# Optimization experiments

Measured on AMD Instinct MI355X. Metric: run time of the kernel, lower is better.

## Reference

```python
import jax, jax.numpy as jnp
import numpy as np
import math

HIDDEN = 1024
NUM_HEADS = 16
HEAD_DIM = HIDDEN // NUM_HEADS
B, S = 4, 1024


def setup_inputs() -> dict:
    key = jax.random.key(0)
    ks = jax.random.split(key, 16)
    sd = 1.0 / math.sqrt(HIDDEN)
    inp = {
        "x": jax.random.normal(ks[0], (B, S, HIDDEN), jnp.float32),
        "spikes": jax.random.uniform(ks[1], (B, S, HIDDEN), jnp.float32),
        "membrane_potential": jax.random.normal(ks[2], (B, S, HIDDEN), jnp.float32),
        "Wq": jax.random.normal(ks[3], (HIDDEN, HIDDEN), jnp.float32) * sd,
        "bq": jnp.zeros((HIDDEN,), jnp.float32),
        "Wk": jax.random.normal(ks[4], (HIDDEN, HIDDEN), jnp.float32) * sd,
        "bk": jnp.zeros((HIDDEN,), jnp.float32),
        "Wv": jax.random.normal(ks[5], (HIDDEN, HIDDEN), jnp.float32) * sd,
        "bv": jnp.zeros((HIDDEN,), jnp.float32),
        "Wo": jax.random.normal(ks[6], (HIDDEN, HIDDEN), jnp.float32) * sd,
        "bo": jnp.zeros((HIDDEN,), jnp.float32),
        "tau_decay": jnp.ones((NUM_HEADS,), jnp.float32) * 10.0,
        "Wg": jax.random.normal(ks[7], (HIDDEN, 2 * HIDDEN), jnp.float32) * sd,
        "bg": jnp.zeros((HIDDEN,), jnp.float32),
    }
    return inp


def _heads(t):  # [B,S,H] -> [B,nH,S,hd]
    Bv, Sv, _ = t.shape
    return t.reshape(Bv, Sv, NUM_HEADS, HEAD_DIM).transpose(0, 2, 1, 3)


def reference(x, spikes, membrane_potential, Wq, bq, Wk, bk, Wv, bv, Wo, bo, tau_decay, Wg, bg):
    scale = 1.0 / math.sqrt(HEAD_DIM)
    q = _heads(x @ Wq.T + bq)
    k = _heads(x @ Wk.T + bk)
    v = _heads(x @ Wv.T + bv)

    # raw scores [B,nH,S,S]
    scores = jnp.einsum('bhqd,bhkd->bhqk', q, k) * scale

    # per-head exponential temporal decay mask [nH,S,S]
    times = jnp.arange(S, dtype=jnp.float32)
    tdiff = jnp.abs(times[:, None] - times[None, :])  # [S,S]
    tmask = jnp.exp(-tdiff[None] / tau_decay[:, None, None])
    scores = scores * tmask[None]

    # spike correlation term
    sm = _heads(spikes)
    spike_attn = jnp.einsum('bhqd,bhkd->bhqk', sm, sm) * scale
    scores = scores * (1.0 + spike_attn)

    # membrane gating of V
    v = v * jax.nn.sigmoid(_heads(membrane_potential))

    probs = jax.nn.softmax(scores, axis=-1)
    context = jnp.einsum('bhqk,bhkd->bhqd', probs, v)
    context = context.transpose(0, 2, 1, 3).reshape(B, S, HIDDEN)

    # dendritic gate
    gate_in = jnp.concatenate([context, membrane_potential], axis=-1)
    gate = jax.nn.sigmoid(gate_in @ Wg.T + bg)
    context = context * gate

    return context @ Wo.T + bo
```

## Files before the change

kernel.cpp:

```cpp
#include <hip/hip_runtime.h>
#include <math.h>
#include <stdint.h>

namespace {

typedef __attribute__((ext_vector_type(8))) short s8v;
typedef __attribute__((ext_vector_type(4))) float f4v;
typedef unsigned short u16;

__device__ __forceinline__ float fexp2(float x) {
  return __builtin_amdgcn_exp2f(x);
}

__device__ __forceinline__ u16 f2bf(float f) {
  union { float f; uint32_t u; } v; v.f = f;
  uint32_t r = v.u + 0x7fffu + ((v.u >> 16) & 1u);
  return (u16)(r >> 16);
}
__device__ __forceinline__ float bf2f(u16 h) {
  union { uint32_t u; float f; } v; v.u = ((uint32_t)h) << 16;
  return v.f;
}
__device__ __forceinline__ uint32_t pk2r(float a, float b) {
  return (uint32_t)f2bf(a) | ((uint32_t)f2bf(b) << 16);
}
__device__ __forceinline__ uint32_t pk2p(float a, float b) {
  union { float f; uint32_t u; } x, y; x.f = a; y.f = b;
  return __builtin_amdgcn_perm(y.u + 0x8000u, x.u + 0x8000u, 0x07060302u);
}
__device__ __forceinline__ float sigmoidf_(float x) { return 1.0f / (1.0f + __expf(-x)); }

__device__ __forceinline__ void gload16(const u16* g, u16* l) {
  __builtin_amdgcn_global_load_lds(
      (const __attribute__((address_space(1))) void*)g,
      (__attribute__((address_space(3))) void*)l, 16, 0, 0);
}

struct CvtJob { const float* src; u16* dst; };
struct CvtArgs { CvtJob j[18]; };

__global__ __launch_bounds__(256) void cvt_kernel(CvtArgs a) {
  const CvtJob jb = a.j[blockIdx.y];
  const int i = blockIdx.x * 256 + threadIdx.x;
  const float4 v = ((const float4*)jb.src)[i];
  uint2 pk;
  pk.x = pk2r(v.x, v.y);
  pk.y = pk2r(v.z, v.w);
  ((uint2*)jb.dst)[i] = pk;
}

__global__ __launch_bounds__(256) void qkv_gemm(
    const u16* __restrict__ xb,
    const u16* __restrict__ Wqb, const u16* __restrict__ Wkb, const u16* __restrict__ Wvb,
    const float* __restrict__ bq, const float* __restrict__ bk, const float* __restrict__ bv,
    const float* __restrict__ mem,
    u16* __restrict__ Qb, u16* __restrict__ Kb, u16* __restrict__ Vt) {
  __shared__ u16 as_[8192], bs_[8192];
  const int t = threadIdx.x;
  const int nb = blockIdx.x, mb = blockIdx.y;
  const int sel = nb >> 3;
  const u16* W = sel == 0 ? Wqb : (sel == 1 ? Wkb : Wvb);
  const float* bias = sel == 0 ? bq : (sel == 1 ? bk : bv);
  const int m0 = mb * 128, n0 = (nb & 7) * 128;
  const f4v fz = {0.f, 0.f, 0.f, 0.f};
  f4v acc[4][4];
#pragma unroll
  for (int i = 0; i < 4; ++i)
#pragma unroll
    for (int j = 0; j < 4; ++j) acc[i][j] = fz;

  const int l = t & 63, w = t >> 6, wm = w >> 1, wn = w & 1;
  const int lr = l & 15, lq = l >> 4;
  const int rx = lr & 7;
  const int srow = t >> 3;
  const int scol = ((t & 7) ^ (srow & 7)) * 8;

#define QKV_STAGE(k0)                                                          \
  {                                                                            \
    const int kk_ = (k0);                                                      \
    _Pragma("unroll") for (int u = 0; u < 4; ++u) {                            \
      gload16(xb + (size_t)(m0 + u * 32 + srow) * 1024 + kk_ + scol,           \
              as_ + u * 2048 + t * 8);                                         \
      gload16(W + (size_t)(n0 + u * 32 + srow) * 1024 + kk_ + scol,            \
              bs_ + u * 2048 + t * 8);                                         \
    }                                                                          \
  }

  QKV_STAGE(0);

  if (sel < 2) {
    for (int c = 0; c < 16; ++c) {
      __syncthreads();
      s8v af[2][4], bf[2][4];
#pragma unroll
      for (int ks = 0; ks < 2; ++ks) {
        const int co = ((ks * 4 + lq) ^ rx) * 8;
#pragma unroll
        for (int mi = 0; mi < 4; ++mi)
          af[ks][mi] = *(const s8v*)(as_ + (wm * 64 + mi * 16 + lr) * 64 + co);
#pragma unroll
        for (int ni = 0; ni < 4; ++ni)
          bf[ks][ni] = *(const s8v*)(bs_ + (wn * 64 + ni * 16 + lr) * 64 + co);
      }
      __syncthreads();
      if (c < 15) QKV_STAGE((c + 1) << 6);
#pragma unroll
      for (int ks = 0; ks < 2; ++ks)
#pragma unroll
        for (int mi = 0; mi < 4; ++mi)
#pragma unroll
          for (int ni = 0; ni < 4; ++ni)
            acc[mi][ni] = __builtin_amdgcn_mfma_f32_16x16x32_bf16(
                bf[ks][ni], af[ks][mi], acc[mi][ni], 0, 0, 0);
    }
    u16* dst = (sel == 0) ? Qb : Kb;
#pragma unroll
    for (int mi = 0; mi < 4; ++mi)
#pragma unroll
      for (int ni = 0; ni < 4; ++ni) {
        const int m = m0 + wm * 64 + mi * 16 + lr;
        const int nb4 = n0 + wn * 64 + ni * 16 + lq * 4;
        const float4 b4 = *(const float4*)&bias[nb4];
        uint2 pk;
        pk.x = pk2r(acc[mi][ni][0] + b4.x, acc[mi][ni][1] + b4.y);
        pk.y = pk2r(acc[mi][ni][2] + b4.z, acc[mi][ni][3] + b4.w);
        *(uint2*)(dst + (size_t)m * 1024 + nb4) = pk;
      }
  } else {
    for (int c = 0; c < 16; ++c) {
      __syncthreads();
      s8v af[2][4], bf[2][4];
#pragma unroll
      for (int ks = 0; ks < 2; ++ks) {
        const int co = ((ks * 4 + lq) ^ rx) * 8;
#pragma unroll
        for (int mi = 0; mi < 4; ++mi)
          af[ks][mi] = *(const s8v*)(as_ + (wm * 64 + mi * 16 + lr) * 64 + co);
#pragma unroll
        for (int ni = 0; ni < 4; ++ni)
          bf[ks][ni] = *(const s8v*)(bs_ + (wn * 64 + ni * 16 + lr) * 64 + co);
      }
      __syncthreads();
      if (c < 15) QKV_STAGE((c + 1) << 6);
#pragma unroll
      for (int ks = 0; ks < 2; ++ks)
#pragma unroll
        for (int mi = 0; mi < 4; ++mi)
#pragma unroll
          for (int ni = 0; ni < 4; ++ni)
            acc[mi][ni] = __builtin_amdgcn_mfma_f32_16x16x32_bf16(
                af[ks][mi], bf[ks][ni], acc[mi][ni], 0, 0, 0);
    }
    const int b = m0 >> 10;
#pragma unroll
    for (int mi = 0; mi < 4; ++mi)
#pragma unroll
      for (int ni = 0; ni < 4; ++ni) {
        const int mrow = m0 + wm * 64 + mi * 16 + lq * 4;
        const int ncol = n0 + wn * 64 + ni * 16 + lr;
        const int h = ncol >> 6, d = ncol & 63;
        const float bi = bias[ncol];
        float tv[4];
#pragma unroll
        for (int r = 0; r < 4; ++r)
          tv[r] = (acc[mi][ni][r] + bi) * sigmoidf_(mem[(size_t)(mrow + r) * 1024 + ncol]);
        const int s = mrow & 1023;
        uint2 pk;
        pk.x = pk2r(tv[0], tv[1]);
        pk.y = pk2r(tv[2], tv[3]);
        *(uint2*)(Vt + ((size_t)((b * 16 + h) * 64 + d)) * 1024 + s) = pk;
      }
  }
#undef QKV_STAGE
}

template <int MODE>
__global__ __launch_bounds__(256) void gemm64(
    const u16* __restrict__ Ab, const u16* __restrict__ A2b,
    const u16* __restrict__ W, const float* __restrict__ bias,
    u16* __restrict__ outb, float* __restrict__ outf, int K) {
  __shared__ u16 as_[4096], bs_[8192];
  const int t = threadIdx.x, l = t & 63, w = t >> 6;
  const int wm = w >> 1, wn = w & 1, lr = l & 15, lq = l >> 4;
  const int m0 = blockIdx.y * 64, n0 = blockIdx.x * 128;
  const f4v fz = {0.f, 0.f, 0.f, 0.f};
  f4v acc[2][4];
#pragma unroll
  for (int i = 0; i < 2; ++i)
#pragma unroll
    for (int j = 0; j < 4; ++j) acc[i][j] = fz;
  const int rx = lr & 7;
  const int srow = t >> 3;
  const int scol = ((t & 7) ^ (srow & 7)) * 8;
  const int nc = K >> 6;

#define G64_STAGE(k0)                                                          \
  {                                                                            \
    const int kk_ = (k0);                                                      \
    const u16* Ae_ = Ab;                                                       \
    int ka_ = kk_;                                                             \
    if (MODE == 1 && kk_ >= 1024) { Ae_ = A2b; ka_ = kk_ - 1024; }             \
    _Pragma("unroll") for (int u = 0; u < 2; ++u)                              \
        gload16(Ae_ + (size_t)(m0 + u * 32 + srow) * 1024 + ka_ + scol,        \
                as_ + u * 2048 + t * 8);                                       \
    _Pragma("unroll") for (int u = 0; u < 4; ++u)                              \
        gload16(W + (size_t)(n0 + u * 32 + srow) * K + kk_ + scol,             \
                bs_ + u * 2048 + t * 8);                                       \
  }

  G64_STAGE(0);
  for (int c = 0; c < nc; ++c) {
    __syncthreads();
    s8v af[2][2], bf[2][4];
#pragma unroll
    for (int ks = 0; ks < 2; ++ks) {
      const int co = ((ks * 4 + lq) ^ rx) * 8;
#pragma unroll
      for (int mi = 0; mi < 2; ++mi)
        af[ks][mi] = *(const s8v*)(as_ + (wm * 32 + mi * 16 + lr) * 64 + co);
#pragma unroll
      for (int ni = 0; ni < 4; ++ni)
        bf[ks][ni] = *(const s8v*)(bs_ + (wn * 64 + ni * 16 + lr) * 64 + co);
    }
    __syncthreads();
    if (c + 1 < nc) G64_STAGE((c + 1) << 6);
#pragma unroll
    for (int ks = 0; ks < 2; ++ks)
#pragma unroll
      for (int mi = 0; mi < 2; ++mi)
#pragma unroll
        for (int ni = 0; ni < 4; ++ni)
          acc[mi][ni] = __builtin_amdgcn_mfma_f32_16x16x32_bf16(
              bf[ks][ni], af[ks][mi], acc[mi][ni], 0, 0, 0);
  }
#undef G64_STAGE

#pragma unroll
  for (int mi = 0; mi < 2; ++mi)
#pragma unroll
    for (int ni = 0; ni < 4; ++ni) {
      const int m = m0 + wm * 32 + mi * 16 + lr;
      const int nb4 = n0 + wn * 64 + ni * 16 + lq * 4;
      const float4 b4 = *(const float4*)&bias[nb4];
      if (MODE == 0) {
        float4 o;
        o.x = acc[mi][ni][0] + b4.x; o.y = acc[mi][ni][1] + b4.y;
        o.z = acc[mi][ni][2] + b4.z; o.w = acc[mi][ni][3] + b4.w;
        *(float4*)(outf + (size_t)m * 1024 + nb4) = o;
      } else {
        const uint2 a2 = *(const uint2*)(Ab + (size_t)m * 1024 + nb4);
        float cx[4] = {bf2f((u16)(a2.x & 0xffff)), bf2f((u16)(a2.x >> 16)),
                       bf2f((u16)(a2.y & 0xffff)), bf2f((u16)(a2.y >> 16))};
        float g[4];
        g[0] = cx[0] * sigmoidf_(acc[mi][ni][0] + b4.x);
        g[1] = cx[1] * sigmoidf_(acc[mi][ni][1] + b4.y);
        g[2] = cx[2] * sigmoidf_(acc[mi][ni][2] + b4.z);
        g[3] = cx[3] * sigmoidf_(acc[mi][ni][3] + b4.w);
        uint2 pk;
        pk.x = pk2r(g[0], g[1]);
        pk.y = pk2r(g[2], g[3]);
        *(uint2*)(outb + (size_t)m * 1024 + nb4) = pk;
      }
    }
}

__global__ __launch_bounds__(256) void attn_mfma(
    const u16* __restrict__ Qb, const u16* __restrict__ Kb,
    const u16* __restrict__ SPb, const u16* __restrict__ Vt,
    const float* __restrict__ tau, u16* __restrict__ CTXb) {
  __shared__ u16 kbuf[8192], skbuf[8192], vbuf[8192];
  __shared__ u16 pbuf[4][1024];
  const int t = threadIdx.x, l = t & 63, w = t >> 6;
  const int lr = l & 15, lq = l >> 4;
  const int pid = blockIdx.x;
  const int g = (pid & 7) + 8 * (pid >> 7);
  const int qt = (pid >> 3) & 15;
  const int h = g & 15, b = g >> 4;

  const float c2 = 1.44269504088896f / tau[h];
  const float K0 = 0.125f * 1.44269504088896f;
  float cNR[4][4], cNRi[4][4];
#pragma unroll
  for (int ni = 0; ni < 4; ++ni)
#pragma unroll
    for (int r = 0; r < 4; ++r) {
      const float d = c2 * (float)(ni * 16 + lq * 4 + r);
      cNR[ni][r]  = fexp2(d);
      cNRi[ni][r] = fexp2(-d);
    }

  s8v qf[2], sf[2];
  {
    const size_t base = ((size_t)(b * 1024 + qt * 64 + w * 16 + lr)) * 1024 + h * 64 + lq * 8;
    qf[0] = *(const s8v*)(Qb + base);
    qf[1] = *(const s8v*)(Qb + base + 32);
    sf[0] = *(const s8v*)(SPb + base);
    sf[1] = *(const s8v*)(SPb + base + 32);
  }
  const s8v ones = {0x3F80, 0x3F80, 0x3F80, 0x3F80, 0x3F80, 0x3F80, 0x3F80, 0x3F80};

  const f4v fz = {0.f, 0.f, 0.f, 0.f};
  f4v oacc[4], osum = fz;
#pragma unroll
  for (int i = 0; i < 4; ++i) oacc[i] = fz;

  const int iqw = qt * 64 + w * 16;
  const int srow = t >> 3;
  const int csw = ((t & 7) ^ (srow & 7)) * 8;
  const int rx = lr & 7;
  u16* pw = pbuf[w];

  auto stage = [&](int jc2, int pp) {
    const int j0s = jc2 * 64;
    const int lo = pp * 4096;
    const size_t kg = ((size_t)(b * 1024 + j0s + srow)) * 1024 + h * 64 + csw;
    gload16(Kb + kg, kbuf + lo + t * 8);
    gload16(Kb + kg + 32 * 1024, kbuf + lo + 2048 + t * 8);
    gload16(SPb + kg, skbuf + lo + t * 8);
    gload16(SPb + kg + 32 * 1024, skbuf + lo + 2048 + t * 8);
    const size_t vg = ((size_t)((b * 16 + h) * 64 + srow)) * 1024 + j0s + csw;
    gload16(Vt + vg, vbuf + lo + t * 8);
    gload16(Vt + vg + 32 * 1024, vbuf + lo + 2048 + t * 8);
  };

  stage(0, 0);
  int pp = 0;
  for (int jc = 0; jc < 16; ++jc) {
    const int j0 = jc * 64;
    __syncthreads();
    if (jc < 15) stage(jc + 1, pp ^ 1);
    const int lo = pp * 4096;

    f4v sa[4], ssa[4];
#pragma unroll
    for (int ni = 0; ni < 4; ++ni) { sa[ni] = fz; ssa[ni] = fz; }
#pragma unroll
    for (int ks = 0; ks < 2; ++ks) {
#pragma unroll
      for (int ni = 0; ni < 4; ++ni) {
        const int off = lo + (ni * 16 + lr) * 64 + (((ks * 4 + lq) ^ rx) * 8);
        const s8v kf = *(const s8v*)(kbuf + off);
        sa[ni] = __builtin_amdgcn_mfma_f32_16x16x32_bf16(kf, qf[ks], sa[ni], 0, 0, 0);
        const s8v skf = *(const s8v*)(skbuf + off);
        ssa[ni] = __builtin_amdgcn_mfma_f32_16x16x32_bf16(skf, sf[ks], ssa[ni], 0, 0, 0);
      }
    }

    const int D0 = iqw - j0;
    float pv[4][4];
    if (jc < qt) {
      const float EA = K0 * fexp2(-c2 * (float)(D0 + lr));
#pragma unroll
      for (int ni = 0; ni < 4; ++ni)
#pragma unroll
        for (int r = 0; r < 4; ++r) {
          const float t1 = fmaf(ssa[ni][r], 0.125f, 1.0f);
          pv[ni][r] = fexp2(sa[ni][r] * (cNR[ni][r] * EA) * t1);
        }
    } else if (jc > qt) {
      const float EAi = K0 * fexp2(c2 * (float)(D0 + lr));
#pragma unroll
      for (int ni = 0; ni < 4; ++ni)
#pragma unroll
        for (int r = 0; r < 4; ++r) {
          const float t1 = fmaf(ssa[ni][r], 0.125f, 1.0f);
          pv[ni][r] = fexp2(sa[ni][r] * (cNRi[ni][r] * EAi) * t1);
        }
    } else {
      const float EA  = K0 * fexp2(-c2 * (float)(D0 + lr));
      const float EAi = K0 * fexp2(c2 * (float)(D0 + lr));
#pragma unroll
      for (int ni = 0; ni < 4; ++ni)
#pragma unroll
        for (int r = 0; r < 4; ++r) {
          const int jloc = ni * 16 + lq * 4 + r;
          const float f = (D0 + lr >= jloc) ? cNR[ni][r] * EA : cNRi[ni][r] * EAi;
          const float t1 = fmaf(ssa[ni][r], 0.125f, 1.0f);
          pv[ni][r] = fexp2(sa[ni][r] * f * t1);
        }
    }

#pragma unroll
    for (int ni = 0; ni < 4; ++ni) {
      const int phys = (ni * 2 + (lq >> 1)) ^ rx;
      uint2 p2;
      p2.x = pk2p(pv[ni][0], pv[ni][1]);
      p2.y = pk2p(pv[ni][2], pv[ni][3]);
      *(uint2*)(pw + lr * 64 + phys * 8 + (lq & 1) * 4) = p2;
    }

#pragma unroll
    for (int ks = 0; ks < 2; ++ks) {
      const s8v pf = *(const s8v*)(pw + lr * 64 + (((ks * 4 + lq) ^ rx) * 8));
      osum = __builtin_amdgcn_mfma_f32_16x16x32_bf16(ones, pf, osum, 0, 0, 0);
#pragma unroll
      for (int nd = 0; nd < 4; ++nd) {
        const int off = lo + (nd * 16 + lr) * 64 + (((ks * 4 + lq) ^ rx) * 8);
        const s8v vf = *(const s8v*)(vbuf + off);
        oacc[nd] = __builtin_amdgcn_mfma_f32_16x16x32_bf16(vf, pf, oacc[nd], 0, 0, 0);
      }
    }
    pp ^= 1;
  }

  const float inv = 1.0f / osum[0];
  const size_t orow = ((size_t)(b * 1024 + qt * 64 + w * 16 + lr)) * 1024 + h * 64;
#pragma unroll
  for (int nd = 0; nd < 4; ++nd) {
    uint2 o;
    o.x = pk2r(oacc[nd][0] * inv, oacc[nd][1] * inv);
    o.y = pk2r(oacc[nd][2] * inv, oacc[nd][3] * inv);
    *(uint2*)(CTXb + orow + nd * 16 + lq * 4) = o;
  }
}

}

extern "C" void kernel_launch(void* const* d_in, const int* in_sizes, int n_in,
                              void* d_out, int out_size, void* d_ws, size_t ws_size,
                              hipStream_t stream) {
  const float* x      = (const float*)d_in[0];
  const float* spikes = (const float*)d_in[1];
  const float* mem    = (const float*)d_in[2];
  const float* Wq     = (const float*)d_in[3];
  const float* bq     = (const float*)d_in[4];
  const float* Wk     = (const float*)d_in[5];
  const float* bk     = (const float*)d_in[6];
  const float* Wv     = (const float*)d_in[7];
  const float* bv     = (const float*)d_in[8];
  const float* Wo     = (const float*)d_in[9];
  const float* bo     = (const float*)d_in[10];
  const float* tau    = (const float*)d_in[11];
  const float* Wg     = (const float*)d_in[12];
  const float* bg     = (const float*)d_in[13];
  float* out = (float*)d_out;

  uint8_t* w8 = (uint8_t*)d_ws;
  u16* spb  = (u16*)(w8);
  u16* xb   = (u16*)(w8 + (8u << 20));
  u16* Wqb  = (u16*)(w8 + (16u << 20));
  u16* Wkb  = (u16*)(w8 + (18u << 20));
  u16* Wvb  = (u16*)(w8 + (20u << 20));
  u16* Wob  = (u16*)(w8 + (22u << 20));
  u16* Wgb  = (u16*)(w8 + (24u << 20));
  u16* Qb   = (u16*)(w8 + (28u << 20));
  u16* Kb   = (u16*)(w8 + (36u << 20));
  u16* Vt   = (u16*)(w8 + (44u << 20));
  u16* CTXb = (u16*)(w8 + (52u << 20));
  u16* memb = (u16*)d_out;
  u16* gctx = xb;

  constexpr size_t QE = 262144 * 4;
  CvtArgs ca;
  for (int q = 0; q < 4; ++q) ca.j[q]     = {x + q * QE,      xb + q * QE};
  for (int q = 0; q < 4; ++q) ca.j[4 + q] = {spikes + q * QE, spb + q * QE};
  for (int q = 0; q < 4; ++q) ca.j[8 + q] = {mem + q * QE,    memb + q * QE};
  ca.j[12] = {Wq, Wqb};
  ca.j[13] = {Wk, Wkb};
  ca.j[14] = {Wv, Wvb};
  ca.j[15] = {Wo, Wob};
  ca.j[16] = {Wg, Wgb};
  ca.j[17] = {Wg + QE, Wgb + QE};
  cvt_kernel<<<dim3(1024, 18), 256, 0, stream>>>(ca);

  qkv_gemm<<<dim3(24, 32), 256, 0, stream>>>(xb, Wqb, Wkb, Wvb, bq, bk, bv, mem,
                                             Qb, Kb, Vt);
  attn_mfma<<<dim3(1024), 256, 0, stream>>>(Qb, Kb, spb, Vt, tau, CTXb);
  gemm64<1><<<dim3(8, 64), 256, 0, stream>>>(CTXb, memb, Wgb, bg, gctx, nullptr, 2048);
  gemm64<0><<<dim3(8, 64), 256, 0, stream>>>(gctx, nullptr, Wob, bo, nullptr, out, 1024);
}
```

Baseline: 272.6 us.

## Process two query tiles per attention block to reuse staged K/V tiles

Each attention workgroup now handles 128 query rows (two 64-row sub-tiles) instead of 64, so every K, spike-K and V tile staged into shared memory feeds twice as many MFMAs. The grid is halved to 512 blocks and the P buffer is doubled. This reduces global/LDS traffic per unit of work, at the cost of more accumulator registers (possibly lower occupancy) and fewer blocks to spread over the CUs.

```diff
diff --git a/kernel.cpp b/kernel.cpp
--- a/kernel.cpp
+++ b/kernel.cpp
@@ -269,12 +269,12 @@
     const u16* __restrict__ SPb, const u16* __restrict__ Vt,
     const float* __restrict__ tau, u16* __restrict__ CTXb) {
   __shared__ u16 kbuf[8192], skbuf[8192], vbuf[8192];
-  __shared__ u16 pbuf[4][1024];
+  __shared__ u16 pbuf[4][2048];
   const int t = threadIdx.x, l = t & 63, w = t >> 6;
   const int lr = l & 15, lq = l >> 4;
   const int pid = blockIdx.x;
-  const int g = (pid & 7) + 8 * (pid >> 7);
-  const int qt = (pid >> 3) & 15;
+  const int g = (pid & 7) + 8 * (pid >> 6);
+  const int qt = (pid >> 3) & 7;
   const int h = g & 15, b = g >> 4;
 
   const float c2 = 1.44269504088896f / tau[h];
@@ -289,22 +289,27 @@
       cNRi[ni][r] = fexp2(-d);
     }
 
-  s8v qf[2], sf[2];
-  {
-    const size_t base = ((size_t)(b * 1024 + qt * 64 + w * 16 + lr)) * 1024 + h * 64 + lq * 8;
-    qf[0] = *(const s8v*)(Qb + base);
-    qf[1] = *(const s8v*)(Qb + base + 32);
-    sf[0] = *(const s8v*)(SPb + base);
-    sf[1] = *(const s8v*)(SPb + base + 32);
+  s8v qf[2][2], sf[2][2];
+#pragma unroll
+  for (int qs = 0; qs < 2; ++qs) {
+    const size_t base =
+        ((size_t)(b * 1024 + qt * 128 + qs * 64 + w * 16 + lr)) * 1024 + h * 64 + lq * 8;
+    qf[qs][0] = *(const s8v*)(Qb + base);
+    qf[qs][1] = *(const s8v*)(Qb + base + 32);
+    sf[qs][0] = *(const s8v*)(SPb + base);
+    sf[qs][1] = *(const s8v*)(SPb + base + 32);
   }
   const s8v ones = {0x3F80, 0x3F80, 0x3F80, 0x3F80, 0x3F80, 0x3F80, 0x3F80, 0x3F80};
 
   const f4v fz = {0.f, 0.f, 0.f, 0.f};
-  f4v oacc[4], osum = fz;
-#pragma unroll
-  for (int i = 0; i < 4; ++i) oacc[i] = fz;
-
-  const int iqw = qt * 64 + w * 16;
+  f4v oacc[2][4], osum[2];
+#pragma unroll
+  for (int qs = 0; qs < 2; ++qs) {
+    osum[qs] = fz;
+#pragma unroll
+    for (int i = 0; i < 4; ++i) oacc[qs][i] = fz;
+  }
+
   const int srow = t >> 3;
   const int csw = ((t & 7) ^ (srow & 7)) * 8;
   const int rx = lr & 7;
@@ -331,86 +336,102 @@
     if (jc < 15) stage(jc + 1, pp ^ 1);
     const int lo = pp * 4096;
 
-    f4v sa[4], ssa[4];
-#pragma unroll
-    for (int ni = 0; ni < 4; ++ni) { sa[ni] = fz; ssa[ni] = fz; }
+    f4v sa[2][4], ssa[2][4];
+#pragma unroll
+    for (int qs = 0; qs < 2; ++qs)
+#pragma unroll
+      for (int ni = 0; ni < 4; ++ni) { sa[qs][ni] = fz; ssa[qs][ni] = fz; }
 #pragma unroll
     for (int ks = 0; ks < 2; ++ks) {
 #pragma unroll
       for (int ni = 0; ni < 4; ++ni) {
         const int off = lo + (ni * 16 + lr) * 64 + (((ks * 4 + lq) ^ rx) * 8);
         const s8v kf = *(const s8v*)(kbuf + off);
-        sa[ni] = __builtin_amdgcn_mfma_f32_16x16x32_bf16(kf, qf[ks], sa[ni], 0, 0, 0);
         const s8v skf = *(const s8v*)(skbuf + off);
-        ssa[ni] = __builtin_amdgcn_mfma_f32_16x16x32_bf16(skf, sf[ks], ssa[ni], 0, 0, 0);
-      }
-    }
-
-    const int D0 = iqw - j0;
-    float pv[4][4];
-    if (jc < qt) {
-      const float EA = K0 * fexp2(-c2 * (float)(D0 + lr));
-#pragma unroll
-      for (int ni = 0; ni < 4; ++ni)
-#pragma unroll
-        for (int r = 0; r < 4; ++r) {
-          const float t1 = fmaf(ssa[ni][r], 0.125f, 1.0f);
-          pv[ni][r] = fexp2(sa[ni][r] * (cNR[ni][r] * EA) * t1);
+#pragma unroll
+        for (int qs = 0; qs < 2; ++qs) {
+          sa[qs][ni] = __builtin_amdgcn_mfma_f32_16x16x32_bf16(kf, qf[qs][ks], sa[qs][ni], 0, 0, 0);
+          ssa[qs][ni] = __builtin_amdgcn_mfma_f32_16x16x32_bf16(skf, sf[qs][ks], ssa[qs][ni], 0, 0, 0);
         }
-    } else if (jc > qt) {
-      const float EAi = K0 * fexp2(c2 * (float)(D0 + lr));
-#pragma unroll
-      for (int ni = 0; ni < 4; ++ni)
-#pragma unroll
-        for (int r = 0; r < 4; ++r) {
-          const float t1 = fmaf(ssa[ni][r], 0.125f, 1.0f);
-          pv[ni][r] = fexp2(sa[ni][r] * (cNRi[ni][r] * EAi) * t1);
-        }
-    } else {
-      const float EA  = K0 * fexp2(-c2 * (float)(D0 + lr));
-      const float EAi = K0 * fexp2(c2 * (float)(D0 + lr));
-#pragma unroll
-      for (int ni = 0; ni < 4; ++ni)
-#pragma unroll
-        for (int r = 0; r < 4; ++r) {
-          const int jloc = ni * 16 + lq * 4 + r;
-          const float f = (D0 + lr >= jloc) ? cNR[ni][r] * EA : cNRi[ni][r] * EAi;
-          const float t1 = fmaf(ssa[ni][r], 0.125f, 1.0f);
-          pv[ni][r] = fexp2(sa[ni][r] * f * t1);
-        }
-    }
-
-#pragma unroll
-    for (int ni = 0; ni < 4; ++ni) {
-      const int phys = (ni * 2 + (lq >> 1)) ^ rx;
-      uint2 p2;
-      p2.x = pk2p(pv[ni][0], pv[ni][1]);
-      p2.y = pk2p(pv[ni][2], pv[ni][3]);
-      *(uint2*)(pw + lr * 64 + phys * 8 + (lq & 1) * 4) = p2;
+      }
+    }
+
+#pragma unroll
+    for (int qs = 0; qs < 2; ++qs) {
+      const int qb = qt * 2 + qs;
+      const int D0 = qb * 64 + w * 16 + lr - j0;
+      float pv[4][4];
+      if (jc < qb) {
+        const float EA = K0 * fexp2(-c2 * (float)D0);
+#pragma unroll
+        for (int ni = 0; ni < 4; ++ni)
+#pragma unroll
+          for (int r = 0; r < 4; ++r) {
+            const float t1 = fmaf(ssa[qs][ni][r], 0.125f, 1.0f);
+            pv[ni][r] = fexp2(sa[qs][ni][r] * (cNR[ni][r] * EA) * t1);
+          }
+      } else if (jc > qb) {
+        const float EAi = K0 * fexp2(c2 * (float)D0);
+#pragma unroll
+        for (int ni = 0; ni < 4; ++ni)
+#pragma unroll
+          for (int r = 0; r < 4; ++r) {
+            const float t1 = fmaf(ssa[qs][ni][r], 0.125f, 1.0f);
+            pv[ni][r] = fexp2(sa[qs][ni][r] * (cNRi[ni][r] * EAi) * t1);
+          }
+      } else {
+        const float EA  = K0 * fexp2(-c2 * (float)D0);
+        const float EAi = K0 * fexp2(c2 * (float)D0);
+#pragma unroll
+        for (int ni = 0; ni < 4; ++ni)
+#pragma unroll
+          for (int r = 0; r < 4; ++r) {
+            const int jloc = ni * 16 + lq * 4 + r;
+            const float f = (D0 >= jloc) ? cNR[ni][r] * EA : cNRi[ni][r] * EAi;
+            const float t1 = fmaf(ssa[qs][ni][r], 0.125f, 1.0f);
+            pv[ni][r] = fexp2(sa[qs][ni][r] * f * t1);
+          }
+      }
+      u16* pq = pw + qs * 1024;
+#pragma unroll
+      for (int ni = 0; ni < 4; ++ni) {
+        const int phys = (ni * 2 + (lq >> 1)) ^ rx;
+        uint2 p2;
+        p2.x = pk2p(pv[ni][0], pv[ni][1]);
+        p2.y = pk2p(pv[ni][2], pv[ni][3]);
+        *(uint2*)(pq + lr * 64 + phys * 8 + (lq & 1) * 4) = p2;
+      }
     }
 
 #pragma unroll
     for (int ks = 0; ks < 2; ++ks) {
-      const s8v pf = *(const s8v*)(pw + lr * 64 + (((ks * 4 + lq) ^ rx) * 8));
-      osum = __builtin_amdgcn_mfma_f32_16x16x32_bf16(ones, pf, osum, 0, 0, 0);
+      const int co = ((ks * 4 + lq) ^ rx) * 8;
+      const s8v pf0 = *(const s8v*)(pw + lr * 64 + co);
+      const s8v pf1 = *(const s8v*)(pw + 1024 + lr * 64 + co);
+      osum[0] = __builtin_amdgcn_mfma_f32_16x16x32_bf16(ones, pf0, osum[0], 0, 0, 0);
+      osum[1] = __builtin_amdgcn_mfma_f32_16x16x32_bf16(ones, pf1, osum[1], 0, 0, 0);
 #pragma unroll
       for (int nd = 0; nd < 4; ++nd) {
-        const int off = lo + (nd * 16 + lr) * 64 + (((ks * 4 + lq) ^ rx) * 8);
-        const s8v vf = *(const s8v*)(vbuf + off);
-        oacc[nd] = __builtin_amdgcn_mfma_f32_16x16x32_bf16(vf, pf, oacc[nd], 0, 0, 0);
+        const s8v vf = *(const s8v*)(vbuf + lo + (nd * 16 + lr) * 64 + co);
+        oacc[0][nd] = __builtin_amdgcn_mfma_f32_16x16x32_bf16(vf, pf0, oacc[0][nd], 0, 0, 0);
+        oacc[1][nd] = __builtin_amdgcn_mfma_f32_16x16x32_bf16(vf, pf1, oacc[1][nd], 0, 0, 0);
       }
     }
     pp ^= 1;
   }
 
-  const float inv = 1.0f / osum[0];
-  const size_t orow = ((size_t)(b * 1024 + qt * 64 + w * 16 + lr)) * 1024 + h * 64;
-#pragma unroll
-  for (int nd = 0; nd < 4; ++nd) {
-    uint2 o;
-    o.x = pk2r(oacc[nd][0] * inv, oacc[nd][1] * inv);
-    o.y = pk2r(oacc[nd][2] * inv, oacc[nd][3] * inv);
-    *(uint2*)(CTXb + orow + nd * 16 + lq * 4) = o;
+#pragma unroll
+  for (int qs = 0; qs < 2; ++qs) {
+    const float inv = 1.0f / osum[qs][0];
+    const size_t orow =
+        ((size_t)(b * 1024 + qt * 128 + qs * 64 + w * 16 + lr)) * 1024 + h * 64;
+#pragma unroll
+    for (int nd = 0; nd < 4; ++nd) {
+      uint2 o;
+      o.x = pk2r(oacc[qs][nd][0] * inv, oacc[qs][nd][1] * inv);
+      o.y = pk2r(oacc[qs][nd][2] * inv, oacc[qs][nd][3] * inv);
+      *(uint2*)(CTXb + orow + nd * 16 + lq * 4) = o;
+    }
   }
 }
 
@@ -465,7 +486,7 @@
 
   qkv_gemm<<<dim3(24, 32), 256, 0, stream>>>(xb, Wqb, Wkb, Wvb, bq, bk, bv, mem,
                                              Qb, Kb, Vt);
-  attn_mfma<<<dim3(1024), 256, 0, stream>>>(Qb, Kb, spb, Vt, tau, CTXb);
+  attn_mfma<<<dim3(512), 256, 0, stream>>>(Qb, Kb, spb, Vt, tau, CTXb);
   gemm64<1><<<dim3(8, 64), 256, 0, stream>>>(CTXb, memb, Wgb, bg, gctx, nullptr, 2048);
   gemm64<0><<<dim3(8, 64), 256, 0, stream>>>(gctx, nullptr, Wob, bo, nullptr, out, 1024);
 }
```

Result: slower. 286.3 us (+5.0%).
